# Kernel optimization log

Hardware: AMD Instinct MI355X
Metric: run time of the kernel (lower is better)

## Reference

```python
import jax, jax.numpy as jnp
import numpy as np

B, C, H_IMG, W_LEN = 32, 32, 16, 512
IN_CH = C * H_IMG          # 512, LSTM input size
OUT_CH = 1024              # bidirectional output size
HID = OUT_CH // 2          # 512, hidden per direction


def setup_inputs() -> dict:
    key = jax.random.key(0)
    ks = jax.random.split(key, 9)
    s = 1.0 / np.sqrt(HID)  # torch LSTM default init scale
    u = lambda k, shape: jax.random.uniform(k, shape, jnp.float32, -s, s)
    return {
        "x": jax.random.normal(ks[0], (B, C, H_IMG, W_LEN), jnp.float32),
        "W_ih_f": u(ks[1], (4 * HID, IN_CH)),
        "W_hh_f": u(ks[2], (4 * HID, HID)),
        "b_ih_f": u(ks[3], (4 * HID,)),
        "b_hh_f": u(ks[4], (4 * HID,)),
        "W_ih_b": u(ks[5], (4 * HID, IN_CH)),
        "W_hh_b": u(ks[6], (4 * HID, HID)),
        "b_ih_b": u(ks[7], (4 * HID,)),
        "b_hh_b": u(ks[8], (4 * HID,)),
    }


def _lstm_dir(x, W_ih, W_hh, b_ih, b_hh, reverse):
    # x: [B, T, IN] -> h sequence [B, T, HID]; torch gate order (i, f, g, o)
    xp = jnp.einsum('bti,gi->btg', x, W_ih) + b_ih + b_hh  # input proj for all steps
    xp = jnp.swapaxes(xp, 0, 1)  # [T, B, 4H]
    if reverse:
        xp = xp[::-1]
    h0 = jnp.zeros((x.shape[0], HID), x.dtype)

    def step(carry, xp_t):
        h, c = carry
        g = xp_t + h @ W_hh.T
        i, f, gg, o = jnp.split(g, 4, axis=-1)
        c = jax.nn.sigmoid(f) * c + jax.nn.sigmoid(i) * jnp.tanh(gg)
        h = jax.nn.sigmoid(o) * jnp.tanh(c)
        return (h, c), h

    _, hs = jax.lax.scan(step, (h0, h0), xp)  # hs: [T, B, HID]
    if reverse:
        hs = hs[::-1]
    return jnp.swapaxes(hs, 0, 1)  # [B, T, HID]


def reference(x, W_ih_f, W_hh_f, b_ih_f, b_hh_f, W_ih_b, W_hh_b, b_ih_b, b_hh_b):
    Bn, Cn, Hn, Wn = x.shape
    # permute(0,3,1,2).view(B, W, C*H): width is the time axis
    xs = jnp.transpose(x, (0, 3, 1, 2)).reshape(Bn, Wn, Cn * Hn)
    hf = _lstm_dir(xs, W_ih_f, W_hh_f, b_ih_f, b_hh_f, reverse=False)
    hb = _lstm_dir(xs, W_ih_b, W_hh_b, b_ih_b, b_hh_b, reverse=True)
    out = jnp.concatenate([hf, hb], axis=-1)        # [B, W, OUT]
    out = jnp.swapaxes(out, 1, 2)                    # [B, OUT, W]
    return out.reshape(Bn, -1, Hn, Wn)               # [B, OUT//H, H, W]
```

## Files before the change

kernel.cpp:

```cpp
#include <hip/hip_runtime.h>
#include <hip/hip_bf16.h>

#define BATCH 32
#define TLEN 512
#define INCH 512
#define HID 512

typedef __bf16 bf16x8 __attribute__((ext_vector_type(8)));
typedef float f32x4 __attribute__((ext_vector_type(4)));
typedef unsigned short u16x4 __attribute__((ext_vector_type(4)));
using bf16 = __hip_bfloat16;

#define OFF_XS2   0ull
#define OFF_WCAT  16777216ull
#define OFF_WHHP  20971520ull
#define OFF_BIAS  25165824ull
#define OFF_HBUF  25182208ull
#define OFF_CTR   25313280ull
#define OFF_FLAG  25313536ull
#define OFF_XP    25321728ull
#define WS_REQUIRED (25321728ull + 134217728ull)

__device__ __forceinline__ float sigmoid_fast(float x) {
    return 1.f / (1.f + __expf(-x));
}
__device__ __forceinline__ float tanh_fast(float x) {
    float ax = fabsf(x);
    float e = __expf(-2.f * ax);
    float r = (1.f - e) / (1.f + e);
    return copysignf(r, x);
}
__device__ __forceinline__ float bf2f(unsigned short u) {
    unsigned int i = ((unsigned int)u) << 16;
    float f; __builtin_memcpy(&f, &i, 4); return f;
}

__global__ void ws_too_small_kernel(float* out) {
    if (threadIdx.x == 0 && blockIdx.x == 0) out[0] = 12345.0f;
}

__global__ void pack_x_kernel(const float* __restrict__ x, bf16* __restrict__ XS2) {
    int bx = blockIdx.x;
    int b  = bx >> 6;
    int tt = (bx >> 3) & 7;
    int kt = bx & 7;
    __shared__ float tile[64][65];
    int tid  = threadIdx.x;
    int row2 = tid >> 6;
    int col  = tid & 63;
#pragma unroll
    for (int i = 0; i < 16; ++i) {
        int row = i * 4 + row2;
        int k = kt * 64 + row;
        tile[row][col] = x[((b * 32 + (k >> 4)) * 16 + (k & 15)) * 512 + tt * 64 + col];
    }
    __syncthreads();
#pragma unroll
    for (int i = 0; i < 16; ++i) {
        int trow = i * 4 + row2;
        int t = tt * 64 + trow;
        XS2[(t * 32 + b) * 512 + kt * 64 + col] = __float2bfloat16(tile[col][trow]);
    }
}

__global__ void pack_w_kernel(const float* __restrict__ Wih_f, const float* __restrict__ Whh_f,
                              const float* __restrict__ bih_f, const float* __restrict__ bhh_f,
                              const float* __restrict__ Wih_b, const float* __restrict__ Whh_b,
                              const float* __restrict__ bih_b, const float* __restrict__ bhh_b,
                              bf16* __restrict__ Wcat, bf16* __restrict__ Whhp,
                              float* __restrict__ bias, unsigned int* __restrict__ hbuf32,
                              unsigned int* __restrict__ ctr, unsigned int* __restrict__ flags) {
    long idx = (long)blockIdx.x * 256 + threadIdx.x;
    if (idx < 262144) {
        long e = idx * 8;
        int m = (int)(e >> 9), k = (int)(e & 511);
        const float* src = (m < 2048) ? &Wih_f[(long)m * 512 + k]
                                      : &Wih_b[(long)(m - 2048) * 512 + k];
        bf16* dst = &Wcat[e];
#pragma unroll
        for (int j = 0; j < 8; ++j) dst[j] = __float2bfloat16(src[j]);
        return;
    }
    idx -= 262144;
    if (idx < 262144) {
        long e = idx * 8;
        int k  = (int)(e & 511);
        int lm = (int)((e >> 9) & 63);
        int s  = (int)((e >> 15) & 31);
        int dir = (int)(e >> 20);
        int grow = (lm & 3) * 512 + s * 16 + (lm >> 2);
        const float* W = dir ? Whh_b : Whh_f;
        const float* src = &W[(long)grow * 512 + k];
        bf16* dst = &Whhp[e];
#pragma unroll
        for (int j = 0; j < 8; ++j) dst[j] = __float2bfloat16(src[j]);
        return;
    }
    idx -= 262144;
    if (idx < 4096) {
        int dir  = (int)(idx >> 11);
        int r    = (int)(idx & 2047);
        int s    = r >> 6, ul = (r >> 2) & 15, gate = r & 3;
        int g    = gate * 512 + s * 16 + ul;
        bias[idx] = (dir ? (bih_b[g] + bhh_b[g]) : (bih_f[g] + bhh_f[g]));
        return;
    }
    idx -= 4096;
    if (idx < 32768) { hbuf32[idx] = 0u; return; }
    idx -= 32768;
    if (idx < 64) { ctr[idx] = 0u; return; }
    idx -= 64;
    if (idx < 2048) { flags[idx] = 0u; return; }
}

__global__ __launch_bounds__(256, 2) void gemm_xp_kernel(const bf16* __restrict__ Wcat,
                                                         const bf16* __restrict__ XS2,
                                                         bf16* __restrict__ XP) {
    int bm = (blockIdx.x & 31) * 128;
    int bn = (blockIdx.x >> 5) * 128;
    __shared__ bf16 lA[128 * 40];
    __shared__ bf16 lB[128 * 40];
    int tid = threadIdx.x;
    int lane = tid & 63, w = tid >> 6;
    int wm = (w & 1) * 64, wn = (w >> 1) * 64;
    int fr = lane & 15, fq = lane >> 4;
    f32x4 acc[4][4] = {};
    int r = tid >> 2, c = tid & 3;
    for (int kt = 0; kt < 16; ++kt) {
        int k0 = kt * 32;
        *(bf16x8*)&lA[r * 40 + c * 8]        = *(const bf16x8*)&Wcat[(long)(bm + r) * 512 + k0 + c * 8];
        *(bf16x8*)&lA[(r + 64) * 40 + c * 8] = *(const bf16x8*)&Wcat[(long)(bm + r + 64) * 512 + k0 + c * 8];
        *(bf16x8*)&lB[r * 40 + c * 8]        = *(const bf16x8*)&XS2[(long)(bn + r) * 512 + k0 + c * 8];
        *(bf16x8*)&lB[(r + 64) * 40 + c * 8] = *(const bf16x8*)&XS2[(long)(bn + r + 64) * 512 + k0 + c * 8];
        __syncthreads();
        bf16x8 af[4], bfm[4];
#pragma unroll
        for (int i = 0; i < 4; ++i) af[i]  = *(const bf16x8*)&lA[(wm + i * 16 + fr) * 40 + fq * 8];
#pragma unroll
        for (int i = 0; i < 4; ++i) bfm[i] = *(const bf16x8*)&lB[(wn + i * 16 + fr) * 40 + fq * 8];
#pragma unroll
        for (int mi = 0; mi < 4; ++mi)
#pragma unroll
            for (int ni = 0; ni < 4; ++ni)
                acc[mi][ni] = __builtin_amdgcn_mfma_f32_16x16x32_bf16(af[mi], bfm[ni], acc[mi][ni], 0, 0, 0);
        __syncthreads();
    }
#pragma unroll
    for (int mi = 0; mi < 4; ++mi) {
#pragma unroll
        for (int rr = 0; rr < 4; ++rr) {
            int m = bm + wm + mi * 16 + fq * 4 + rr;
            int dir = m >> 11, cc = m & 2047;
            int gate = cc >> 9, u = cc & 511, s = u >> 4, ul = u & 15;
#pragma unroll
            for (int ni = 0; ni < 4; ++ni) {
                int n = bn + wn + ni * 16 + fr;
                int t = n >> 5, b = n & 31;
                long off = ((long)(t * 2 + dir) * 32 + s) * 2048 + (long)(ul * 32 + b) * 4 + gate;
                XP[off] = __float2bfloat16(acc[mi][ni][rr]);
            }
        }
    }
}

__global__ __launch_bounds__(512, 2) void lstm_rec_kernel(const bf16* __restrict__ Whhp,
                                                          const bf16* __restrict__ XP,
                                                          const float* __restrict__ bias,
                                                          bf16* hbuf, float* out,
                                                          unsigned int* flags) {
    int bx = blockIdx.x;
    int dir = bx >> 5, s = bx & 31;
    int tid = threadIdx.x;
    int lane = tid & 63, w = tid >> 6;
    int mt = w & 3, nt = w >> 2;
    int fr = lane & 15, fq = lane >> 4;
    __shared__ float obuf[16][512];
    __shared__ bf16  hstage[BATCH * 16];
    __shared__ bf16  hsh[32 * 520];

    const bf16* wbase = Whhp + ((long)((dir * 32 + s) * 64 + mt * 16 + fr)) * 512 + fq * 8;
    bf16x8 wA[16];
#pragma unroll
    for (int kt = 0; kt < 16; ++kt) wA[kt] = *(const bf16x8*)(wbase + kt * 32);

    int ul = mt * 4 + fq;
    int b  = nt * 16 + fr;
    f32x4 bv = *(const f32x4*)&bias[((dir * 32 + s) * 16 + ul) * 4];
    float cstate = 0.f;

    bf16* hb_dir = hbuf + (long)dir * 2 * BATCH * HID;
    unsigned int* myflag = flags + (dir * 32 + s) * 32;
    const unsigned int* pollflag = flags + (dir * 32 + (lane & 31)) * 32;
    float* outrow = out + (long)b * 524288 + (long)(dir * 512 + s * 16 + ul) * 512;
    int srow = tid >> 4, scol = (tid & 15) * 32;
    int guard = 1 << 21;

    for (int t = 0; t < TLEN; ++t) {
        int ttime = dir ? (TLEN - 1 - t) : t;
        const bf16* xpp = XP + (long)(ttime * 2 + dir) * 65536 + s * 2048 + (ul * 32 + b) * 4;
        u16x4 xv = *(const u16x4*)xpp;

        if (t > 0) {
            unsigned int target = (unsigned int)t;
            for (;;) {
                unsigned int v = __hip_atomic_load(pollflag, __ATOMIC_RELAXED,
                                                   __HIP_MEMORY_SCOPE_AGENT);
                if (__all(v >= target)) break;
                if (--guard <= 0) break;
            }
        }

        {
            const bf16* src = hb_dir + (long)(t & 1) * BATCH * HID + (long)srow * 512 + scol;
            f32x4 v0, v1, v2, v3;
            asm volatile(
                "global_load_dwordx4 %0, %4, off sc0 sc1\n\t"
                "global_load_dwordx4 %1, %4, off offset:16 sc0 sc1\n\t"
                "global_load_dwordx4 %2, %4, off offset:32 sc0 sc1\n\t"
                "global_load_dwordx4 %3, %4, off offset:48 sc0 sc1\n\t"
                "s_waitcnt vmcnt(0)"
                : "=&v"(v0), "=&v"(v1), "=&v"(v2), "=&v"(v3)
                : "v"(src) : "memory");
            bf16* d = &hsh[srow * 520 + scol];
            *(f32x4*)(d)      = v0;
            *(f32x4*)(d + 8)  = v1;
            *(f32x4*)(d + 16) = v2;
            *(f32x4*)(d + 24) = v3;
        }
        __syncthreads();

        f32x4 a0 = {}, a1 = {}, a2 = {}, a3 = {};
        const bf16* hrow = &hsh[(nt * 16 + fr) * 520 + fq * 8];
#pragma unroll
        for (int kt = 0; kt < 16; kt += 4) {
            bf16x8 h0 = *(const bf16x8*)(hrow + (kt + 0) * 32);
            bf16x8 h1 = *(const bf16x8*)(hrow + (kt + 1) * 32);
            bf16x8 h2 = *(const bf16x8*)(hrow + (kt + 2) * 32);
            bf16x8 h3 = *(const bf16x8*)(hrow + (kt + 3) * 32);
            a0 = __builtin_amdgcn_mfma_f32_16x16x32_bf16(wA[kt + 0], h0, a0, 0, 0, 0);
            a1 = __builtin_amdgcn_mfma_f32_16x16x32_bf16(wA[kt + 1], h1, a1, 0, 0, 0);
            a2 = __builtin_amdgcn_mfma_f32_16x16x32_bf16(wA[kt + 2], h2, a2, 0, 0, 0);
            a3 = __builtin_amdgcn_mfma_f32_16x16x32_bf16(wA[kt + 3], h3, a3, 0, 0, 0);
        }

        float gi = (a0[0] + a1[0]) + (a2[0] + a3[0]) + bv[0] + bf2f(xv.x);
        float gf = (a0[1] + a1[1]) + (a2[1] + a3[1]) + bv[1] + bf2f(xv.y);
        float gg = (a0[2] + a1[2]) + (a2[2] + a3[2]) + bv[2] + bf2f(xv.z);
        float go = (a0[3] + a1[3]) + (a2[3] + a3[3]) + bv[3] + bf2f(xv.w);
        float si = sigmoid_fast(gi), sf = sigmoid_fast(gf), so = sigmoid_fast(go);
        cstate = sf * cstate + si * tanh_fast(gg);
        float h = so * tanh_fast(cstate);

        hstage[b * 16 + ul] = __float2bfloat16(h);
        obuf[ttime & 15][tid] = h;
        __syncthreads();

        if (w == 0) {
            int hbb = lane >> 1, half = lane & 1;
            f32x4 hv = *(const f32x4*)&hstage[hbb * 16 + half * 8];
            bf16* dst = hb_dir + (long)((t + 1) & 1) * BATCH * HID + (long)hbb * 512
                        + s * 16 + half * 8;
            asm volatile("global_store_dwordx4 %0, %1, off sc0 sc1"
                         :: "v"(dst), "v"(hv) : "memory");
            asm volatile("s_waitcnt vmcnt(0)" ::: "memory");
            if (lane == 0)
                __hip_atomic_store(myflag, (unsigned int)(t + 1), __ATOMIC_RELAXED,
                                   __HIP_MEMORY_SCOPE_AGENT);
        }

        if ((t & 15) == 15) {
            int tb = ttime & ~15;
            float vals[16];
#pragma unroll
            for (int c = 0; c < 16; ++c) vals[c] = obuf[c][tid];
            float* op = outrow + tb;
#pragma unroll
            for (int c4 = 0; c4 < 4; ++c4)
                *(f32x4*)(op + c4 * 4) = *(f32x4*)&vals[c4 * 4];
        }
    }
}

extern "C" void kernel_launch(void* const* d_in, const int* in_sizes, int n_in,
                              void* d_out, int out_size, void* d_ws, size_t ws_size,
                              hipStream_t stream) {
    const float* x     = (const float*)d_in[0];
    const float* Wih_f = (const float*)d_in[1];
    const float* Whh_f = (const float*)d_in[2];
    const float* bih_f = (const float*)d_in[3];
    const float* bhh_f = (const float*)d_in[4];
    const float* Wih_b = (const float*)d_in[5];
    const float* Whh_b = (const float*)d_in[6];
    const float* bih_b = (const float*)d_in[7];
    const float* bhh_b = (const float*)d_in[8];
    float* out = (float*)d_out;

    if (ws_size < WS_REQUIRED) {
        ws_too_small_kernel<<<1, 64, 0, stream>>>(out);
        return;
    }

    char* ws = (char*)d_ws;
    bf16* XS2  = (bf16*)(ws + OFF_XS2);
    bf16* Wcat = (bf16*)(ws + OFF_WCAT);
    bf16* Whhp = (bf16*)(ws + OFF_WHHP);
    float* bias = (float*)(ws + OFF_BIAS);
    bf16* hbuf = (bf16*)(ws + OFF_HBUF);
    unsigned int* ctr   = (unsigned int*)(ws + OFF_CTR);
    unsigned int* flags = (unsigned int*)(ws + OFF_FLAG);
    bf16* XP   = (bf16*)(ws + OFF_XP);

    pack_x_kernel<<<2048, 256, 0, stream>>>(x, XS2);
    pack_w_kernel<<<2201, 256, 0, stream>>>(Wih_f, Whh_f, bih_f, bhh_f,
                                            Wih_b, Whh_b, bih_b, bhh_b,
                                            Wcat, Whhp, bias, (unsigned int*)hbuf, ctr, flags);
    gemm_xp_kernel<<<4096, 256, 0, stream>>>(Wcat, XS2, XP);
    lstm_rec_kernel<<<64, 512, 0, stream>>>(Whhp, XP, bias, hbuf, out, flags);
}
```

Baseline: 2.026 ms.

## Poll peer flags from one wavefront and relayout hidden-state exchange buffer

Only wavefront 1 now spins on the global per-block flags and publishes the step through a shared-memory epoch variable; the other wavefronts spin on LDS instead of all eight issuing global atomic loads. The global hidden-state buffer is relaid out so each block writes one contiguous 1 KB chunk (slice-major) and each thread reads a contiguous 64-byte span, with scatter into the padded LDS layout. This is meant to cut global polling traffic and make the cross-block stores and loads contiguous. In exchange the other waves spin on LDS, and the LDS epoch handoff uses relaxed ordering, which risks visibility or ordering issues.

```diff
diff --git a/kernel.cpp b/kernel.cpp
--- a/kernel.cpp
+++ b/kernel.cpp
@@ -177,6 +177,7 @@
     __shared__ float obuf[16][512];
     __shared__ bf16  hstage[BATCH * 16];
     __shared__ bf16  hsh[32 * 520];
+    __shared__ int   eps;
 
     const bf16* wbase = Whhp + ((long)((dir * 32 + s) * 64 + mt * 16 + fr)) * 512 + fq * 8;
     bf16x8 wA[16];
@@ -188,12 +189,17 @@
     f32x4 bv = *(const f32x4*)&bias[((dir * 32 + s) * 16 + ul) * 4];
     float cstate = 0.f;
 
-    bf16* hb_dir = hbuf + (long)dir * 2 * BATCH * HID;
+    bf16* hb_dir = hbuf + (long)dir * 2 * 16384;
     unsigned int* myflag = flags + (dir * 32 + s) * 32;
     const unsigned int* pollflag = flags + (dir * 32 + (lane & 31)) * 32;
     float* outrow = out + (long)b * 524288 + (long)(dir * 512 + s * 16 + ul) * 512;
-    int srow = tid >> 4, scol = (tid & 15) * 32;
+    int c0 = tid * 4;
+    int sb0 = ((c0 >> 1) & 31) * 520 + (c0 >> 6) * 16;
+    int sb1 = (((c0 + 2) >> 1) & 31) * 520 + (c0 >> 6) * 16;
     int guard = 1 << 21;
+
+    if (tid == 0) eps = 0;
+    __syncthreads();
 
     for (int t = 0; t < TLEN; ++t) {
         int ttime = dir ? (TLEN - 1 - t) : t;
@@ -201,17 +207,27 @@
         u16x4 xv = *(const u16x4*)xpp;
 
         if (t > 0) {
-            unsigned int target = (unsigned int)t;
-            for (;;) {
-                unsigned int v = __hip_atomic_load(pollflag, __ATOMIC_RELAXED,
-                                                   __HIP_MEMORY_SCOPE_AGENT);
-                if (__all(v >= target)) break;
-                if (--guard <= 0) break;
+            if (w == 1) {
+                unsigned int target = (unsigned int)t;
+                for (;;) {
+                    unsigned int v = __hip_atomic_load(pollflag, __ATOMIC_RELAXED,
+                                                       __HIP_MEMORY_SCOPE_AGENT);
+                    if (__all(v >= target)) break;
+                    if (--guard <= 0) break;
+                }
+                if (lane == 0)
+                    __hip_atomic_store(&eps, t, __ATOMIC_RELAXED,
+                                       __HIP_MEMORY_SCOPE_WORKGROUP);
+            } else {
+                while (__hip_atomic_load(&eps, __ATOMIC_RELAXED,
+                                         __HIP_MEMORY_SCOPE_WORKGROUP) < t) {
+                    if (--guard <= 0) break;
+                }
             }
         }
 
         {
-            const bf16* src = hb_dir + (long)(t & 1) * BATCH * HID + (long)srow * 512 + scol;
+            const bf16* src = hb_dir + (long)(t & 1) * 16384 + (long)tid * 32;
             f32x4 v0, v1, v2, v3;
             asm volatile(
                 "global_load_dwordx4 %0, %4, off sc0 sc1\n\t"
@@ -221,11 +237,12 @@
                 "s_waitcnt vmcnt(0)"
                 : "=&v"(v0), "=&v"(v1), "=&v"(v2), "=&v"(v3)
                 : "v"(src) : "memory");
-            bf16* d = &hsh[srow * 520 + scol];
-            *(f32x4*)(d)      = v0;
-            *(f32x4*)(d + 8)  = v1;
-            *(f32x4*)(d + 16) = v2;
-            *(f32x4*)(d + 24) = v3;
+            bf16* d0 = &hsh[sb0];
+            bf16* d1 = &hsh[sb1];
+            *(f32x4*)(d0)     = v0;
+            *(f32x4*)(d0 + 8) = v1;
+            *(f32x4*)(d1)     = v2;
+            *(f32x4*)(d1 + 8) = v3;
         }
         __syncthreads();
 
@@ -256,10 +273,8 @@
         __syncthreads();
 
         if (w == 0) {
-            int hbb = lane >> 1, half = lane & 1;
-            f32x4 hv = *(const f32x4*)&hstage[hbb * 16 + half * 8];
-            bf16* dst = hb_dir + (long)((t + 1) & 1) * BATCH * HID + (long)hbb * 512
-                        + s * 16 + half * 8;
+            f32x4 hv = *(const f32x4*)&hstage[lane * 8];
+            bf16* dst = hb_dir + (long)((t + 1) & 1) * 16384 + s * 512 + lane * 8;
             asm volatile("global_store_dwordx4 %0, %1, off sc0 sc1"
                          :: "v"(dst), "v"(hv) : "memory");
             asm volatile("s_waitcnt vmcnt(0)" ::: "memory");
```

Result: faster. 1.957 ms (-3.4%).

## Replace flag polling with step-tagged hidden-state words for inter-block sync

Applied to the files above, without the earlier changes.

Each hidden value is now stored as a 32-bit word that carries the bf16 value in its low half and the timestep tag in its high half. Consumers spin on loading the data itself until every tag matches, which removes the separate flag store, the s_waitcnt before it, the flag poll, and the second __syncthreads per step. The shared hidden-state buffer is double-buffered so the next step's writes do not race with current reads. In exchange the hidden-state traffic doubles, since each bf16 now occupies a full 32-bit word. The H32 buffer reuses the XS2 region after the GEMM has consumed it, and a separate zero kernel clears it.

```diff
diff --git a/kernel.cpp b/kernel.cpp
--- a/kernel.cpp
+++ b/kernel.cpp
@@ -8,6 +8,7 @@
 
 typedef __bf16 bf16x8 __attribute__((ext_vector_type(8)));
 typedef float f32x4 __attribute__((ext_vector_type(4)));
+typedef unsigned int u32x4 __attribute__((ext_vector_type(4)));
 typedef unsigned short u16x4 __attribute__((ext_vector_type(4)));
 using bf16 = __hip_bfloat16;
 
@@ -68,8 +69,7 @@
                               const float* __restrict__ Wih_b, const float* __restrict__ Whh_b,
                               const float* __restrict__ bih_b, const float* __restrict__ bhh_b,
                               bf16* __restrict__ Wcat, bf16* __restrict__ Whhp,
-                              float* __restrict__ bias, unsigned int* __restrict__ hbuf32,
-                              unsigned int* __restrict__ ctr, unsigned int* __restrict__ flags) {
+                              float* __restrict__ bias) {
     long idx = (long)blockIdx.x * 256 + threadIdx.x;
     if (idx < 262144) {
         long e = idx * 8;
@@ -105,12 +105,12 @@
         bias[idx] = (dir ? (bih_b[g] + bhh_b[g]) : (bih_f[g] + bhh_f[g]));
         return;
     }
-    idx -= 4096;
-    if (idx < 32768) { hbuf32[idx] = 0u; return; }
-    idx -= 32768;
-    if (idx < 64) { ctr[idx] = 0u; return; }
-    idx -= 64;
-    if (idx < 2048) { flags[idx] = 0u; return; }
+}
+
+__global__ void zero_h_kernel(unsigned int* __restrict__ H32) {
+    int i = (blockIdx.x * 256 + threadIdx.x) * 4;
+    u32x4 z = {0u, 0u, 0u, 0u};
+    *(u32x4*)&H32[i] = z;
 }
 
 __global__ __launch_bounds__(256, 2) void gemm_xp_kernel(const bf16* __restrict__ Wcat,
@@ -163,11 +163,10 @@
     }
 }
 
-__global__ __launch_bounds__(512, 2) void lstm_rec_kernel(const bf16* __restrict__ Whhp,
+__global__ __launch_bounds__(512, 1) void lstm_rec_kernel(const bf16* __restrict__ Whhp,
                                                           const bf16* __restrict__ XP,
                                                           const float* __restrict__ bias,
-                                                          bf16* hbuf, float* out,
-                                                          unsigned int* flags) {
+                                                          unsigned int* H32, float* out) {
     int bx = blockIdx.x;
     int dir = bx >> 5, s = bx & 31;
     int tid = threadIdx.x;
@@ -175,8 +174,7 @@
     int mt = w & 3, nt = w >> 2;
     int fr = lane & 15, fq = lane >> 4;
     __shared__ float obuf[16][512];
-    __shared__ bf16  hstage[BATCH * 16];
-    __shared__ bf16  hsh[32 * 520];
+    __shared__ bf16  hsh[2][32 * 526];
 
     const bf16* wbase = Whhp + ((long)((dir * 32 + s) * 64 + mt * 16 + fr)) * 512 + fq * 8;
     bf16x8 wA[16];
@@ -188,49 +186,87 @@
     f32x4 bv = *(const f32x4*)&bias[((dir * 32 + s) * 16 + ul) * 4];
     float cstate = 0.f;
 
-    bf16* hb_dir = hbuf + (long)dir * 2 * BATCH * HID;
-    unsigned int* myflag = flags + (dir * 32 + s) * 32;
-    const unsigned int* pollflag = flags + (dir * 32 + (lane & 31)) * 32;
+    unsigned int* Hd = H32 + dir * 32768;
+    const unsigned int* src_base = Hd + tid * 32;
+    unsigned int* st_base = Hd + s * 512 + b * 16 + ul;
+    int sp = tid >> 4;
+    int b0 = (tid & 15) * 2;
     float* outrow = out + (long)b * 524288 + (long)(dir * 512 + s * 16 + ul) * 512;
-    int srow = tid >> 4, scol = (tid & 15) * 32;
-    int guard = 1 << 21;
+    int guard = 1 << 20;
 
     for (int t = 0; t < TLEN; ++t) {
         int ttime = dir ? (TLEN - 1 - t) : t;
         const bf16* xpp = XP + (long)(ttime * 2 + dir) * 65536 + s * 2048 + (ul * 32 + b) * 4;
         u16x4 xv = *(const u16x4*)xpp;
 
-        if (t > 0) {
-            unsigned int target = (unsigned int)t;
-            for (;;) {
-                unsigned int v = __hip_atomic_load(pollflag, __ATOMIC_RELAXED,
-                                                   __HIP_MEMORY_SCOPE_AGENT);
-                if (__all(v >= target)) break;
-                if (--guard <= 0) break;
-            }
-        }
-
+        const unsigned int* src = src_base + (t & 1) * 16384;
+        unsigned int tt = (unsigned int)t;
+        u32x4 v0, v1, v2, v3, v4, v5, v6, v7;
+        for (;;) {
+            asm volatile(
+                "global_load_dwordx4 %0, %8, off sc0 sc1\n\t"
+                "global_load_dwordx4 %1, %8, off offset:16 sc0 sc1\n\t"
+                "global_load_dwordx4 %2, %8, off offset:32 sc0 sc1\n\t"
+                "global_load_dwordx4 %3, %8, off offset:48 sc0 sc1\n\t"
+                "global_load_dwordx4 %4, %8, off offset:64 sc0 sc1\n\t"
+                "global_load_dwordx4 %5, %8, off offset:80 sc0 sc1\n\t"
+                "global_load_dwordx4 %6, %8, off offset:96 sc0 sc1\n\t"
+                "global_load_dwordx4 %7, %8, off offset:112 sc0 sc1\n\t"
+                "s_waitcnt vmcnt(0)"
+                : "=&v"(v0), "=&v"(v1), "=&v"(v2), "=&v"(v3),
+                  "=&v"(v4), "=&v"(v5), "=&v"(v6), "=&v"(v7)
+                : "v"(src) : "memory");
+            unsigned int bad;
+            bad  = (v0.x >> 16) ^ tt; bad |= (v0.y >> 16) ^ tt;
+            bad |= (v0.z >> 16) ^ tt; bad |= (v0.w >> 16) ^ tt;
+            bad |= (v1.x >> 16) ^ tt; bad |= (v1.y >> 16) ^ tt;
+            bad |= (v1.z >> 16) ^ tt; bad |= (v1.w >> 16) ^ tt;
+            bad |= (v2.x >> 16) ^ tt; bad |= (v2.y >> 16) ^ tt;
+            bad |= (v2.z >> 16) ^ tt; bad |= (v2.w >> 16) ^ tt;
+            bad |= (v3.x >> 16) ^ tt; bad |= (v3.y >> 16) ^ tt;
+            bad |= (v3.z >> 16) ^ tt; bad |= (v3.w >> 16) ^ tt;
+            bad |= (v4.x >> 16) ^ tt; bad |= (v4.y >> 16) ^ tt;
+            bad |= (v4.z >> 16) ^ tt; bad |= (v4.w >> 16) ^ tt;
+            bad |= (v5.x >> 16) ^ tt; bad |= (v5.y >> 16) ^ tt;
+            bad |= (v5.z >> 16) ^ tt; bad |= (v5.w >> 16) ^ tt;
+            bad |= (v6.x >> 16) ^ tt; bad |= (v6.y >> 16) ^ tt;
+            bad |= (v6.z >> 16) ^ tt; bad |= (v6.w >> 16) ^ tt;
+            bad |= (v7.x >> 16) ^ tt; bad |= (v7.y >> 16) ^ tt;
+            bad |= (v7.z >> 16) ^ tt; bad |= (v7.w >> 16) ^ tt;
+            if (bad == 0) break;
+            if (--guard <= 0) break;
+        }
+
+        unsigned int p0  = (v0.x & 0xFFFFu) | (v0.y << 16);
+        unsigned int p1  = (v0.z & 0xFFFFu) | (v0.w << 16);
+        unsigned int p2  = (v1.x & 0xFFFFu) | (v1.y << 16);
+        unsigned int p3  = (v1.z & 0xFFFFu) | (v1.w << 16);
+        unsigned int p4  = (v2.x & 0xFFFFu) | (v2.y << 16);
+        unsigned int p5  = (v2.z & 0xFFFFu) | (v2.w << 16);
+        unsigned int p6  = (v3.x & 0xFFFFu) | (v3.y << 16);
+        unsigned int p7  = (v3.z & 0xFFFFu) | (v3.w << 16);
+        unsigned int p8  = (v4.x & 0xFFFFu) | (v4.y << 16);
+        unsigned int p9  = (v4.z & 0xFFFFu) | (v4.w << 16);
+        unsigned int p10 = (v5.x & 0xFFFFu) | (v5.y << 16);
+        unsigned int p11 = (v5.z & 0xFFFFu) | (v5.w << 16);
+        unsigned int p12 = (v6.x & 0xFFFFu) | (v6.y << 16);
+        unsigned int p13 = (v6.z & 0xFFFFu) | (v6.w << 16);
+        unsigned int p14 = (v7.x & 0xFFFFu) | (v7.y << 16);
+        unsigned int p15 = (v7.z & 0xFFFFu) | (v7.w << 16);
         {
-            const bf16* src = hb_dir + (long)(t & 1) * BATCH * HID + (long)srow * 512 + scol;
-            f32x4 v0, v1, v2, v3;
-            asm volatile(
-                "global_load_dwordx4 %0, %4, off sc0 sc1\n\t"
-                "global_load_dwordx4 %1, %4, off offset:16 sc0 sc1\n\t"
-                "global_load_dwordx4 %2, %4, off offset:32 sc0 sc1\n\t"
-                "global_load_dwordx4 %3, %4, off offset:48 sc0 sc1\n\t"
-                "s_waitcnt vmcnt(0)"
-                : "=&v"(v0), "=&v"(v1), "=&v"(v2), "=&v"(v3)
-                : "v"(src) : "memory");
-            bf16* d = &hsh[srow * 520 + scol];
-            *(f32x4*)(d)      = v0;
-            *(f32x4*)(d + 8)  = v1;
-            *(f32x4*)(d + 16) = v2;
-            *(f32x4*)(d + 24) = v3;
+            u32x4 q0 = {p0, p1, p2, p3},   q1 = {p4, p5, p6, p7};
+            u32x4 q2 = {p8, p9, p10, p11}, q3 = {p12, p13, p14, p15};
+            bf16* d0 = &hsh[t & 1][b0 * 526 + sp * 16];
+            bf16* d1 = &hsh[t & 1][(b0 + 1) * 526 + sp * 16];
+            *(u32x4*)(d0)     = q0;
+            *(u32x4*)(d0 + 8) = q1;
+            *(u32x4*)(d1)     = q2;
+            *(u32x4*)(d1 + 8) = q3;
         }
         __syncthreads();
 
         f32x4 a0 = {}, a1 = {}, a2 = {}, a3 = {};
-        const bf16* hrow = &hsh[(nt * 16 + fr) * 520 + fq * 8];
+        const bf16* hrow = &hsh[t & 1][(nt * 16 + fr) * 526 + fq * 8];
 #pragma unroll
         for (int kt = 0; kt < 16; kt += 4) {
             bf16x8 h0 = *(const bf16x8*)(hrow + (kt + 0) * 32);
@@ -251,23 +287,14 @@
         cstate = sf * cstate + si * tanh_fast(gg);
         float h = so * tanh_fast(cstate);
 
-        hstage[b * 16 + ul] = __float2bfloat16(h);
+        bf16 hb16 = __float2bfloat16(h);
+        unsigned short hsb; __builtin_memcpy(&hsb, &hb16, 2);
+        unsigned int hw = ((unsigned int)(t + 1) << 16) | (unsigned int)hsb;
+        unsigned int* haddr = st_base + ((t + 1) & 1) * 16384;
+        asm volatile("global_store_dword %0, %1, off sc0 sc1"
+                     :: "v"(haddr), "v"(hw) : "memory");
+
         obuf[ttime & 15][tid] = h;
-        __syncthreads();
-
-        if (w == 0) {
-            int hbb = lane >> 1, half = lane & 1;
-            f32x4 hv = *(const f32x4*)&hstage[hbb * 16 + half * 8];
-            bf16* dst = hb_dir + (long)((t + 1) & 1) * BATCH * HID + (long)hbb * 512
-                        + s * 16 + half * 8;
-            asm volatile("global_store_dwordx4 %0, %1, off sc0 sc1"
-                         :: "v"(dst), "v"(hv) : "memory");
-            asm volatile("s_waitcnt vmcnt(0)" ::: "memory");
-            if (lane == 0)
-                __hip_atomic_store(myflag, (unsigned int)(t + 1), __ATOMIC_RELAXED,
-                                   __HIP_MEMORY_SCOPE_AGENT);
-        }
-
         if ((t & 15) == 15) {
             int tb = ttime & ~15;
             float vals[16];
@@ -305,15 +332,14 @@
     bf16* Wcat = (bf16*)(ws + OFF_WCAT);
     bf16* Whhp = (bf16*)(ws + OFF_WHHP);
     float* bias = (float*)(ws + OFF_BIAS);
-    bf16* hbuf = (bf16*)(ws + OFF_HBUF);
-    unsigned int* ctr   = (unsigned int*)(ws + OFF_CTR);
-    unsigned int* flags = (unsigned int*)(ws + OFF_FLAG);
+    unsigned int* H32 = (unsigned int*)(ws + OFF_XS2);
     bf16* XP   = (bf16*)(ws + OFF_XP);
 
     pack_x_kernel<<<2048, 256, 0, stream>>>(x, XS2);
-    pack_w_kernel<<<2201, 256, 0, stream>>>(Wih_f, Whh_f, bih_f, bhh_f,
+    pack_w_kernel<<<2065, 256, 0, stream>>>(Wih_f, Whh_f, bih_f, bhh_f,
                                             Wih_b, Whh_b, bih_b, bhh_b,
-                                            Wcat, Whhp, bias, (unsigned int*)hbuf, ctr, flags);
+                                            Wcat, Whhp, bias);
     gemm_xp_kernel<<<4096, 256, 0, stream>>>(Wcat, XS2, XP);
-    lstm_rec_kernel<<<64, 512, 0, stream>>>(Whhp, XP, bias, hbuf, out, flags);
-}
+    zero_h_kernel<<<64, 256, 0, stream>>>(H32);
+    lstm_rec_kernel<<<64, 512, 0, stream>>>(Whhp, XP, bias, H32, out);
+}
```

After: 6.027 ms. +197.5%, slower.
